# Kernel optimization log

Measured on AMD Instinct MI355X. Metric: run time of the kernel, lower is better.

Reference implementation:

```python
import jax, jax.numpy as jnp
import numpy as np


def _hamilton_weight(Wr, Wi, Wj, Wk):
    # Weights stored as [in4, out4] (i.e. torch weight.T). Build the fused
    # block-structured quaternion matrix [in, out]; rows = input chunk (r,i,j,k),
    # cols = output chunk (r,i,j,k), signs per the Hamilton product in forward().
    return jnp.concatenate([
        jnp.concatenate([Wr,  Wi,  Wj,  Wk], axis=1),
        jnp.concatenate([-Wi, Wr,  Wk, -Wj], axis=1),
        jnp.concatenate([-Wj, -Wk, Wr,  Wi], axis=1),
        jnp.concatenate([-Wk, Wj, -Wi,  Wr], axis=1),
    ], axis=0)


def _hamilton_bias(br, bi, bj, bk):
    # Each output chunk sums the four linears' biases with the same signs.
    return jnp.concatenate([
        br - bi - bj - bk,
        br + bi + bj - bk,
        br - bi + bj + bk,
        br + bi - bj + bk,
    ], axis=0)


def setup_inputs() -> dict:
    key = jax.random.key(0)
    ks = jax.random.split(key, 9)
    B, IN, OUT = 8192, 4096, 4096
    q_in, q_out = IN // 4, OUT // 4
    s = 1.0 / np.sqrt(q_in)
    return {
        "x": jax.random.normal(ks[0], (B, IN), dtype=jnp.float32),
        "Wr": jax.random.normal(ks[1], (q_in, q_out), dtype=jnp.float32) * s,
        "Wi": jax.random.normal(ks[2], (q_in, q_out), dtype=jnp.float32) * s,
        "Wj": jax.random.normal(ks[3], (q_in, q_out), dtype=jnp.float32) * s,
        "Wk": jax.random.normal(ks[4], (q_in, q_out), dtype=jnp.float32) * s,
        "br": jax.random.normal(ks[5], (q_out,), dtype=jnp.float32) * s,
        "bi": jax.random.normal(ks[6], (q_out,), dtype=jnp.float32) * s,
        "bj": jax.random.normal(ks[7], (q_out,), dtype=jnp.float32) * s,
        "bk": jax.random.normal(ks[8], (q_out,), dtype=jnp.float32) * s,
    }


def reference(x, Wr, Wi, Wj, Wk, br, bi, bj, bk):
    # Single fused GEMM; mathematically identical to the 16 small matmuls
    # (r/i/j/k linears applied to each chunk with Hamilton-product signs)
    # followed by concat.
    W = _hamilton_weight(Wr, Wi, Wj, Wk)   # [in, out]
    b = _hamilton_bias(br, bi, bj, bk)     # [out]
    return x @ W + b
```

## Files before the change

### kernel.cpp

```cpp
#include <hip/hip_runtime.h>
#include <stdint.h>

#define MDIM 8192
#define NDIM 4096
#define KDIM 4096

typedef float accf_t __attribute__((ext_vector_type(4)));
typedef short s16x8 __attribute__((ext_vector_type(8)));

typedef const __attribute__((address_space(1))) uint8_t* gas_t;
typedef __attribute__((address_space(3))) uint8_t* las_t;

__device__ __forceinline__ void gload16(const void* g, void* l) {
  __builtin_amdgcn_global_load_lds((gas_t)g, (las_t)l, 16, 0, 0);
}

__device__ __forceinline__ uint32_t pk_bf16(float a, float b) {
  uint32_t ua = __builtin_bit_cast(uint32_t, a);
  uint32_t ub = __builtin_bit_cast(uint32_t, b);
  ua += 0x7fffu + ((ua >> 16) & 1u);
  ub += 0x7fffu + ((ub >> 16) & 1u);
  return (ua >> 16) | (ub & 0xffff0000u);
}

__global__ void cvt_x_kernel(const float* __restrict__ x, uint16_t* __restrict__ xb) {
  int64_t e = ((int64_t)blockIdx.x * 256 + threadIdx.x) * 8;
  float4 f0 = *reinterpret_cast<const float4*>(x + e);
  float4 f1 = *reinterpret_cast<const float4*>(x + e + 4);
  uint4 u;
  u.x = pk_bf16(f0.x, f0.y);
  u.y = pk_bf16(f0.z, f0.w);
  u.z = pk_bf16(f1.x, f1.y);
  u.w = pk_bf16(f1.z, f1.w);
  *reinterpret_cast<uint4*>(xb + e) = u;
}

__global__ void build_wt_kernel(const float* __restrict__ Wr, const float* __restrict__ Wi,
                                const float* __restrict__ Wj, const float* __restrict__ Wk,
                                uint16_t* __restrict__ wt) {
  __shared__ float t[64][65];
  const int k0 = blockIdx.x * 64;
  const int n0 = blockIdx.y * 64;
  const int rc = k0 >> 10, cc = n0 >> 10;
  const int srcsel[16] = {0,1,2,3, 1,0,3,2, 2,3,0,1, 3,2,1,0};
  const float sgntab[16] = {1.f,1.f,1.f,1.f, -1.f,1.f,1.f,-1.f, -1.f,-1.f,1.f,1.f, -1.f,1.f,-1.f,1.f};
  const float* srcs[4] = {Wr, Wi, Wj, Wk};
  const float* W = srcs[srcsel[rc * 4 + cc]];
  const float sg = sgntab[rc * 4 + cc];
  const int kq0 = k0 & 1023, nq0 = n0 & 1023;
  const int tid = threadIdx.x;
  const int lr = tid >> 6;
  const int lc = tid & 63;
#pragma unroll
  for (int p = 0; p < 16; ++p) {
    int kl = p * 4 + lr;
    t[kl][lc] = W[(int64_t)(kq0 + kl) * 1024 + nq0 + lc];
  }
  __syncthreads();
  const int kb = (tid & 7) * 8;
#pragma unroll
  for (int p = 0; p < 2; ++p) {
    int nl = p * 32 + (tid >> 3);
    uint4 u;
    u.x = pk_bf16(sg * t[kb + 0][nl], sg * t[kb + 1][nl]);
    u.y = pk_bf16(sg * t[kb + 2][nl], sg * t[kb + 3][nl]);
    u.z = pk_bf16(sg * t[kb + 4][nl], sg * t[kb + 5][nl]);
    u.w = pk_bf16(sg * t[kb + 6][nl], sg * t[kb + 7][nl]);
    *reinterpret_cast<uint4*>(wt + (int64_t)(n0 + nl) * KDIM + k0 + kb) = u;
  }
}


#define VM6 { asm volatile("s_waitcnt vmcnt(6)"); __builtin_amdgcn_sched_barrier(0); }
#define VM0 { asm volatile("s_waitcnt vmcnt(0)"); __builtin_amdgcn_sched_barrier(0); }

#define ISS(BUF, H, T) {                                                      \
    int64_t ko_ = (int64_t)(T) * 64 + ((H) >> 1) * 32;                        \
    const uint16_t* s0_ = ((H) & 1) ? bSrc0 : aSrc0;                          \
    const uint16_t* s1_ = ((H) & 1) ? bSrc1 : aSrc1;                          \
    uint8_t* d_ = dstW + (BUF) * 65536 + (H) * 16384;                         \
    gload16(s0_ + ko_, d_);                                                   \
    gload16(s1_ + ko_, d_ + 8192); }

#define PH(BUF, KH, MH, ISSUE, LASTVM)                                        \
  {                                                                           \
    if ((MH) == 0) {                                                          \
      _Pragma("unroll")                                                       \
      for (int f = 0; f < 4; ++f)                                             \
        bfr[f] = *(const s16x8*)(ldsb + (BUF) * 65536 + (KH) * 32768 + boff[f]); \
    }                                                                         \
    s16x8 afr[4];                                                             \
    _Pragma("unroll")                                                         \
    for (int f = 0; f < 4; ++f)                                               \
      afr[f] = *(const s16x8*)(ldsb + (BUF) * 65536 + (KH) * 32768 + aoff[(MH) * 4 + f]); \
    ISSUE                                                                     \
    __builtin_amdgcn_s_barrier();                                             \
    asm volatile("s_waitcnt lgkmcnt(0)");                                     \
    __builtin_amdgcn_sched_barrier(0);                                        \
    __builtin_amdgcn_s_setprio(1);                                            \
    _Pragma("unroll")                                                         \
    for (int f = 0; f < 4; ++f)                                               \
      _Pragma("unroll")                                                       \
      for (int fn = 0; fn < 4; ++fn)                                          \
        acc[(MH) * 4 + f][fn] =                                               \
            __builtin_amdgcn_mfma_f32_16x16x32_bf16(afr[f], bfr[fn], acc[(MH) * 4 + f][fn], 0, 0, 0); \
    __builtin_amdgcn_s_setprio(0);                                            \
    LASTVM                                                                    \
    __builtin_amdgcn_s_barrier();                                             \
  }

__global__ __launch_bounds__(512, 2)
void qgemm8_kernel(const uint16_t* __restrict__ xb, const uint16_t* __restrict__ wt,
                   const float* __restrict__ br, const float* __restrict__ bi,
                   const float* __restrict__ bj, const float* __restrict__ bk,
                   float* __restrict__ out) {
  extern __shared__ uint8_t ldsb[];
  const int tid = threadIdx.x;
  const int wid = tid >> 6, lane = tid & 63;
  const int kg = lane >> 4, rl = lane & 15;
  const int wm = wid >> 2, wn = wid & 3;

  const int bid = blockIdx.x;
  const int swz = (bid & 7) * 64 + (bid >> 3);
  const int tn = swz >> 5, tm = swz & 31;
  const int m0 = tm * 256, n0 = tn * 256;

  const int arow = tid >> 2, aslot = tid & 3;
  const int ag = aslot ^ ((arow >> 1) & 3);
  const uint16_t* aSrc0 = xb + (int64_t)(m0 + arow) * KDIM + ag * 8;
  const uint16_t* aSrc1 = xb + (int64_t)(m0 + 128 + arow) * KDIM + ag * 8;
  const uint16_t* bSrc0 = wt + (int64_t)(n0 + arow) * KDIM + ag * 8;
  const uint16_t* bSrc1 = wt + (int64_t)(n0 + 128 + arow) * KDIM + ag * 8;
  uint8_t* dstW = ldsb + wid * 1024;

  int aoff[8], boff[4];
#pragma unroll
  for (int f = 0; f < 8; ++f) {
    int r = wm * 128 + f * 16 + rl;
    aoff[f] = r * 64 + ((kg ^ ((r >> 1) & 3)) << 4);
  }
#pragma unroll
  for (int f = 0; f < 4; ++f) {
    int c = wn * 64 + f * 16 + rl;
    boff[f] = 16384 + c * 64 + ((kg ^ ((c >> 1) & 3)) << 4);
  }

  accf_t acc[8][4] = {};
  s16x8 bfr[4];

  ISS(0, 0, 0) ISS(0, 1, 0) ISS(0, 2, 0) ISS(0, 3, 0)
  ISS(1, 0, 1) ISS(1, 1, 1) ISS(1, 2, 1)
  VM6
  __builtin_amdgcn_s_barrier();

  for (int i = 0; i < 31; ++i) {
    const int t = 2 * i;
    PH(0, 0, 0, ISS(1, 3, t + 1), )
    PH(0, 0, 1, ISS(0, 0, t + 2), )
    PH(0, 1, 0, ISS(0, 1, t + 2), )
    PH(0, 1, 1, ISS(0, 2, t + 2), VM6)
    PH(1, 0, 0, ISS(0, 3, t + 2), )
    PH(1, 0, 1, ISS(1, 0, t + 3), )
    PH(1, 1, 0, ISS(1, 1, t + 3), )
    PH(1, 1, 1, ISS(1, 2, t + 3), VM6)
  }
  PH(0, 0, 0, ISS(1, 3, 63), )
  PH(0, 0, 1, , )
  PH(0, 1, 0, , )
  PH(0, 1, 1, , VM0)
  PH(1, 0, 0, , )
  PH(1, 0, 1, , )
  PH(1, 1, 0, , )
  PH(1, 1, 1, , )

  const float s_i[4] = {-1.f, 1.f, -1.f, 1.f};
  const float s_j[4] = {-1.f, 1.f, 1.f, -1.f};
  const float s_k[4] = {-1.f, -1.f, 1.f, 1.f};
  float bias[4];
#pragma unroll
  for (int fn = 0; fn < 4; ++fn) {
    int col = n0 + wn * 64 + fn * 16 + rl;
    int cc = col >> 10, nq = col & 1023;
    bias[fn] = br[nq] + s_i[cc] * bi[nq] + s_j[cc] * bj[nq] + s_k[cc] * bk[nq];
  }
#pragma unroll
  for (int fm = 0; fm < 8; ++fm) {
    int rowb = m0 + wm * 128 + fm * 16 + kg * 4;
#pragma unroll
    for (int r = 0; r < 4; ++r) {
      float* op = out + (int64_t)(rowb + r) * NDIM + n0 + wn * 64 + rl;
#pragma unroll
      for (int fn = 0; fn < 4; ++fn)
        op[fn * 16] = acc[fm][fn][r] + bias[fn];
    }
  }
}

template <int AWS>
__global__ __launch_bounds__(256, 3)
void qgemm_kernel(const uint16_t* __restrict__ xb, const float* __restrict__ xf,
                  const uint16_t* __restrict__ wt,
                  const float* __restrict__ br, const float* __restrict__ bi,
                  const float* __restrict__ bj, const float* __restrict__ bk,
                  float* __restrict__ out) {
  __shared__ __align__(16) uint16_t Alds[128 * 32];
  __shared__ __align__(16) uint16_t Blds[128 * 32];
  const int tid = threadIdx.x;
  const int wid = tid >> 6, lane = tid & 63;
  const int kg = lane >> 4, rl = lane & 15;
  const int bid = blockIdx.x;
  const int swz = (bid & 7) * 256 + (bid >> 3);
  const int tile_m = swz & 63;
  const int tile_n = swz >> 6;
  const int m0 = tile_m * 128, n0 = tile_n * 128;
  const int wr = wid >> 1, wc = wid & 1;
  const int e0 = tid * 8, e1 = (256 + tid) * 8;
  const int r0 = e0 >> 5, r1 = e1 >> 5;
  const int s0 = (e0 >> 3) & 3, s1 = (e1 >> 3) & 3;
  const int g0 = s0 ^ ((r0 >> 1) & 3);
  const int g1 = s1 ^ ((r1 >> 1) & 3);
  const uint16_t* bp0 = wt + (int64_t)(n0 + r0) * KDIM + g0 * 8;
  const uint16_t* bp1 = wt + (int64_t)(n0 + r1) * KDIM + g1 * 8;
  const uint16_t* ap0 = nullptr;
  const uint16_t* ap1 = nullptr;
  const float* af0 = nullptr;
  const float* af1 = nullptr;
  if (AWS) {
    ap0 = xb + (int64_t)(m0 + r0) * KDIM + g0 * 8;
    ap1 = xb + (int64_t)(m0 + r1) * KDIM + g1 * 8;
  } else {
    af0 = xf + (int64_t)(m0 + r0) * KDIM + g0 * 8;
    af1 = xf + (int64_t)(m0 + r1) * KDIM + g1 * 8;
  }
  uint8_t* Ab = (uint8_t*)Alds;
  uint8_t* Bb = (uint8_t*)Blds;
  uint8_t* AbW0 = Ab + wid * 1024;
  uint8_t* AbW1 = Ab + 4096 + wid * 1024;
  uint8_t* BbW0 = Bb + wid * 1024;
  uint8_t* BbW1 = Bb + 4096 + wid * 1024;
  uint8_t* aw0 = Ab + e0 * 2;
  uint8_t* aw1 = Ab + e1 * 2;
  int aoff[4], boff[4];
#pragma unroll
  for (int f = 0; f < 4; ++f) {
    int arow = wr * 64 + f * 16 + rl;
    aoff[f] = arow * 64 + ((kg ^ ((arow >> 1) & 3)) << 4);
    int bcol = wc * 64 + f * 16 + rl;
    boff[f] = bcol * 64 + ((kg ^ ((bcol >> 1) & 3)) << 4);
  }
  accf_t acc[4][4] = {};
  for (int kt = 0; kt < KDIM / 32; ++kt) {
    gload16(bp0, BbW0);
    gload16(bp1, BbW1);
    bp0 += 32; bp1 += 32;
    if (AWS) {
      gload16(ap0, AbW0);
      gload16(ap1, AbW1);
      ap0 += 32; ap1 += 32;
    } else {
      float4 fa = *reinterpret_cast<const float4*>(af0);
      float4 fb = *reinterpret_cast<const float4*>(af0 + 4);
      float4 fc = *reinterpret_cast<const float4*>(af1);
      float4 fd = *reinterpret_cast<const float4*>(af1 + 4);
      uint4 u0, u1;
      u0.x = pk_bf16(fa.x, fa.y); u0.y = pk_bf16(fa.z, fa.w);
      u0.z = pk_bf16(fb.x, fb.y); u0.w = pk_bf16(fb.z, fb.w);
      u1.x = pk_bf16(fc.x, fc.y); u1.y = pk_bf16(fc.z, fc.w);
      u1.z = pk_bf16(fd.x, fd.y); u1.w = pk_bf16(fd.z, fd.w);
      *reinterpret_cast<uint4*>(aw0) = u0;
      *reinterpret_cast<uint4*>(aw1) = u1;
      af0 += 32; af1 += 32;
    }
    __syncthreads();
    s16x8 afr[4], bfr[4];
#pragma unroll
    for (int f = 0; f < 4; ++f) afr[f] = *reinterpret_cast<const s16x8*>(Ab + aoff[f]);
#pragma unroll
    for (int f = 0; f < 4; ++f) bfr[f] = *reinterpret_cast<const s16x8*>(Bb + boff[f]);
#pragma unroll
    for (int fm = 0; fm < 4; ++fm)
#pragma unroll
      for (int fn = 0; fn < 4; ++fn)
        acc[fm][fn] = __builtin_amdgcn_mfma_f32_16x16x32_bf16(afr[fm], bfr[fn], acc[fm][fn], 0, 0, 0);
    __syncthreads();
  }
  const float s_i[4] = {-1.f, 1.f, -1.f, 1.f};
  const float s_j[4] = {-1.f, 1.f, 1.f, -1.f};
  const float s_k[4] = {-1.f, -1.f, 1.f, 1.f};
  float bias[4];
#pragma unroll
  for (int fn = 0; fn < 4; ++fn) {
    int col = n0 + wc * 64 + fn * 16 + rl;
    int cc = col >> 10, nq = col & 1023;
    bias[fn] = br[nq] + s_i[cc] * bi[nq] + s_j[cc] * bj[nq] + s_k[cc] * bk[nq];
  }
#pragma unroll
  for (int fm = 0; fm < 4; ++fm) {
    int rowb = m0 + wr * 64 + fm * 16 + kg * 4;
#pragma unroll
    for (int r = 0; r < 4; ++r) {
      float* op = out + (int64_t)(rowb + r) * NDIM + n0 + wc * 64 + rl;
#pragma unroll
      for (int fn = 0; fn < 4; ++fn)
        op[fn * 16] = acc[fm][fn][r] + bias[fn];
    }
  }
}

__global__ void naive_q_kernel(const float* __restrict__ x,
                               const float* __restrict__ Wr, const float* __restrict__ Wi,
                               const float* __restrict__ Wj, const float* __restrict__ Wk,
                               const float* __restrict__ br, const float* __restrict__ bi,
                               const float* __restrict__ bj, const float* __restrict__ bk,
                               float* __restrict__ out) {
  const int n = blockIdx.x * 256 + threadIdx.x;
  const int m = blockIdx.y;
  const int cc = n >> 10, nq = n & 1023;
  const int srcsel[16] = {0,1,2,3, 1,0,3,2, 2,3,0,1, 3,2,1,0};
  const float sgntab[16] = {1.f,1.f,1.f,1.f, -1.f,1.f,1.f,-1.f, -1.f,-1.f,1.f,1.f, -1.f,1.f,-1.f,1.f};
  const float s_i[4] = {-1.f,1.f,-1.f,1.f}, s_j[4] = {-1.f,1.f,1.f,-1.f}, s_k[4] = {-1.f,-1.f,1.f,1.f};
  const float* srcs[4] = {Wr, Wi, Wj, Wk};
  float acc = br[nq] + s_i[cc] * bi[nq] + s_j[cc] * bj[nq] + s_k[cc] * bk[nq];
  for (int rc = 0; rc < 4; ++rc) {
    const float* W = srcs[srcsel[rc * 4 + cc]];
    const float sg = sgntab[rc * 4 + cc];
    const float* xp = x + (int64_t)m * KDIM + rc * 1024;
    const float* wp = W + nq;
    float a = 0.f;
    for (int kq = 0; kq < 1024; ++kq) a = fmaf(xp[kq], wp[(int64_t)kq * 1024], a);
    acc += sg * a;
  }
  out[(int64_t)m * NDIM + n] = acc;
}

extern "C" void kernel_launch(void* const* d_in, const int* in_sizes, int n_in,
                              void* d_out, int out_size, void* d_ws, size_t ws_size,
                              hipStream_t stream) {
  const float* x  = (const float*)d_in[0];
  const float* Wr = (const float*)d_in[1];
  const float* Wi = (const float*)d_in[2];
  const float* Wj = (const float*)d_in[3];
  const float* Wk = (const float*)d_in[4];
  const float* br = (const float*)d_in[5];
  const float* bi = (const float*)d_in[6];
  const float* bj = (const float*)d_in[7];
  const float* bk = (const float*)d_in[8];
  float* out = (float*)d_out;

  const size_t WT_BYTES = (size_t)NDIM * KDIM * 2;
  const size_t XB_BYTES = (size_t)MDIM * KDIM * 2;

  if (ws_size < WT_BYTES) {
    dim3 g(NDIM / 256, MDIM);
    naive_q_kernel<<<g, 256, 0, stream>>>(x, Wr, Wi, Wj, Wk, br, bi, bj, bk, out);
    return;
  }
  uint16_t* wt = (uint16_t*)d_ws;
  build_wt_kernel<<<dim3(64, 64), 256, 0, stream>>>(Wr, Wi, Wj, Wk, wt);
  if (ws_size >= WT_BYTES + XB_BYTES) {
    uint16_t* xbp = wt + (size_t)NDIM * KDIM;
    cvt_x_kernel<<<(MDIM * (KDIM / 8)) / 256, 256, 0, stream>>>(x, xbp);
    hipError_t e = hipFuncSetAttribute(reinterpret_cast<const void*>(qgemm8_kernel),
                                       hipFuncAttributeMaxDynamicSharedMemorySize, 131072);
    if (e == hipSuccess) {
      qgemm8_kernel<<<512, 512, 131072, stream>>>(xbp, wt, br, bi, bj, bk, out);
    } else {
      qgemm_kernel<1><<<2048, 256, 0, stream>>>(xbp, nullptr, wt, br, bi, bj, bk, out);
    }
  } else {
    qgemm_kernel<0><<<2048, 256, 0, stream>>>(nullptr, x, wt, br, bi, bj, bk, out);
  }
}
```

Baseline: 311.4 us.

## Double-buffer LDS fragment registers to prefetch next phase during MFMA

Restructures the main loop phases so that the A and B fragments for the next phase are loaded from LDS into a second register set while the current phase's MFMAs run. Partial lgkmcnt waits replace full drains, and global-load waits move to finer vmcnt(10) checks at the top of each phase. The aim is to hide LDS read latency behind matrix math. The cost is higher VGPR pressure from the doubled fragment arrays, under a 512-thread, 2-block launch bound. The waitcnt accounting is more delicate and could be wrong.

After: 313.8 us. No clear change (+0.8%).

```diff
diff --git a/kernel.cpp b/kernel.cpp
--- a/kernel.cpp
+++ b/kernel.cpp
@@ -71,8 +71,10 @@
 }
 
 
-#define VM6 { asm volatile("s_waitcnt vmcnt(6)"); __builtin_amdgcn_sched_barrier(0); }
-#define VM0 { asm volatile("s_waitcnt vmcnt(0)"); __builtin_amdgcn_sched_barrier(0); }
+#define SB __builtin_amdgcn_sched_barrier(0);
+#define W10 { asm volatile("s_waitcnt vmcnt(10)"); SB }
+#define WV0 { asm volatile("s_waitcnt vmcnt(0)"); SB }
+#define NOW
 
 #define ISS(BUF, H, T) {                                                      \
     int64_t ko_ = (int64_t)(T) * 64 + ((H) >> 1) * 32;                        \
@@ -82,30 +84,30 @@
     gload16(s0_ + ko_, d_);                                                   \
     gload16(s1_ + ko_, d_ + 8192); }
 
-#define PH(BUF, KH, MH, ISSUE, LASTVM)                                        \
+#define PH2(BUF, KH, MH, CA, NA, CB, LB, NB, NBUF, NKH, NMH, LGK, ISSUE, TOPW) \
   {                                                                           \
-    if ((MH) == 0) {                                                          \
+    ISSUE                                                                     \
+    __builtin_amdgcn_s_barrier();                                             \
+    TOPW                                                                      \
+    _Pragma("unroll")                                                         \
+    for (int f = 0; f < 4; ++f)                                               \
+      afr[NA][f] = *(const s16x8*)(ldsb + (NBUF) * 65536 + (NKH) * 32768 + aoff[(NMH) * 4 + f]); \
+    if (LB) {                                                                 \
       _Pragma("unroll")                                                       \
       for (int f = 0; f < 4; ++f)                                             \
-        bfr[f] = *(const s16x8*)(ldsb + (BUF) * 65536 + (KH) * 32768 + boff[f]); \
+        bfr[NB][f] = *(const s16x8*)(ldsb + (NBUF) * 65536 + (NKH) * 32768 + boff[f]); \
     }                                                                         \
-    s16x8 afr[4];                                                             \
-    _Pragma("unroll")                                                         \
-    for (int f = 0; f < 4; ++f)                                               \
-      afr[f] = *(const s16x8*)(ldsb + (BUF) * 65536 + (KH) * 32768 + aoff[(MH) * 4 + f]); \
-    ISSUE                                                                     \
-    __builtin_amdgcn_s_barrier();                                             \
-    asm volatile("s_waitcnt lgkmcnt(0)");                                     \
-    __builtin_amdgcn_sched_barrier(0);                                        \
+    SB                                                                        \
+    asm volatile("s_waitcnt lgkmcnt(" LGK ")");                               \
+    SB                                                                        \
     __builtin_amdgcn_s_setprio(1);                                            \
     _Pragma("unroll")                                                         \
     for (int f = 0; f < 4; ++f)                                               \
       _Pragma("unroll")                                                       \
       for (int fn = 0; fn < 4; ++fn)                                          \
         acc[(MH) * 4 + f][fn] =                                               \
-            __builtin_amdgcn_mfma_f32_16x16x32_bf16(afr[f], bfr[fn], acc[(MH) * 4 + f][fn], 0, 0, 0); \
+            __builtin_amdgcn_mfma_f32_16x16x32_bf16(afr[CA][f], bfr[CB][fn], acc[(MH) * 4 + f][fn], 0, 0, 0); \
     __builtin_amdgcn_s_setprio(0);                                            \
-    LASTVM                                                                    \
     __builtin_amdgcn_s_barrier();                                             \
   }
 
@@ -146,32 +148,39 @@
   }
 
   accf_t acc[8][4] = {};
-  s16x8 bfr[4];
+  s16x8 afr[2][4], bfr[2][4];
 
   ISS(0, 0, 0) ISS(0, 1, 0) ISS(0, 2, 0) ISS(0, 3, 0)
   ISS(1, 0, 1) ISS(1, 1, 1) ISS(1, 2, 1)
-  VM6
+  { asm volatile("s_waitcnt vmcnt(6)"); SB }
   __builtin_amdgcn_s_barrier();
+#pragma unroll
+  for (int f = 0; f < 4; ++f)
+    afr[0][f] = *(const s16x8*)(ldsb + aoff[f]);
+#pragma unroll
+  for (int f = 0; f < 4; ++f)
+    bfr[0][f] = *(const s16x8*)(ldsb + boff[f]);
+  SB
 
   for (int i = 0; i < 31; ++i) {
     const int t = 2 * i;
-    PH(0, 0, 0, ISS(1, 3, t + 1), )
-    PH(0, 0, 1, ISS(0, 0, t + 2), )
-    PH(0, 1, 0, ISS(0, 1, t + 2), )
-    PH(0, 1, 1, ISS(0, 2, t + 2), VM6)
-    PH(1, 0, 0, ISS(0, 3, t + 2), )
-    PH(1, 0, 1, ISS(1, 0, t + 3), )
-    PH(1, 1, 0, ISS(1, 1, t + 3), )
-    PH(1, 1, 1, ISS(1, 2, t + 3), VM6)
-  }
-  PH(0, 0, 0, ISS(1, 3, 63), )
-  PH(0, 0, 1, , )
-  PH(0, 1, 0, , )
-  PH(0, 1, 1, , VM0)
-  PH(1, 0, 0, , )
-  PH(1, 0, 1, , )
-  PH(1, 1, 0, , )
-  PH(1, 1, 1, , )
+    PH2(0,  0, 0,  0, 1, 0, 0, 0,  0,   0,  1,   "4", ISS(1, 3, t + 1), W10)
+    PH2(0,  0, 1,  1, 0, 0, 1, 1,  0,   1,  0,   "8", ISS(0, 0, t + 2), W10)
+    PH2(0,  1, 0,  0, 1, 1, 0, 0,  0,   1,  1,   "4", ISS(0, 1, t + 2), W10)
+    PH2(0,  1, 1,  1, 0, 1, 1, 0,  1,   0,  0,   "8", ISS(0, 2, t + 2), W10)
+    PH2(1,  0, 0,  0, 1, 0, 0, 0,  1,   0,  1,   "4", ISS(0, 3, t + 2), W10)
+    PH2(1,  0, 1,  1, 0, 0, 1, 1,  1,   1,  0,   "8", ISS(1, 0, t + 3), W10)
+    PH2(1,  1, 0,  0, 1, 1, 0, 0,  1,   1,  1,   "4", ISS(1, 1, t + 3), W10)
+    PH2(1,  1, 1,  1, 0, 1, 1, 0,  0,   0,  0,   "8", ISS(1, 2, t + 3), W10)
+  }
+  PH2(0, 0, 0,  0, 1, 0, 0, 0,  0, 0, 1,  "4", ISS(1, 3, 63), W10)
+  PH2(0, 0, 1,  1, 0, 0, 1, 1,  0, 1, 0,  "8", NOW, WV0)
+  PH2(0, 1, 0,  0, 1, 1, 0, 0,  0, 1, 1,  "4", NOW, NOW)
+  PH2(0, 1, 1,  1, 0, 1, 1, 0,  1, 0, 0,  "8", NOW, NOW)
+  PH2(1, 0, 0,  0, 1, 0, 0, 0,  1, 0, 1,  "4", NOW, NOW)
+  PH2(1, 0, 1,  1, 0, 0, 1, 1,  1, 1, 0,  "8", NOW, NOW)
+  PH2(1, 1, 0,  0, 1, 1, 0, 0,  1, 1, 1,  "4", NOW, NOW)
+  PH2(1, 1, 1,  1, 0, 1, 1, 0,  0, 0, 0,  "8", NOW, NOW)
 
   const float s_i[4] = {-1.f, 1.f, -1.f, 1.f};
   const float s_j[4] = {-1.f, 1.f, 1.f, -1.f};
```

## Split main GEMM into two M-half launches and reorder LDS load issue

Applied to the files above, without the earlier changes.

Launches the 512-thread GEMM kernel twice, each covering half of the M rows via a new mbase argument and a retuned block swizzle. It also reorders the per-phase global-to-LDS issue sequence and moves the B-offset constant into the LDS read macro. The aim appears to be a smaller per-launch working set for better cache locality and a different load ordering. The risk is that each launch fills fewer occupancy slots and adds a serial launch boundary. The fallback kernel's template variant is also removed.

Result: faster. 295.1 us (-5.2%).

```diff
diff --git a/kernel.cpp b/kernel.cpp
--- a/kernel.cpp
+++ b/kernel.cpp
@@ -71,8 +71,9 @@
 }
 
 
-#define VM6 { asm volatile("s_waitcnt vmcnt(6)"); __builtin_amdgcn_sched_barrier(0); }
-#define VM0 { asm volatile("s_waitcnt vmcnt(0)"); __builtin_amdgcn_sched_barrier(0); }
+#define SB __builtin_amdgcn_sched_barrier(0);
+#define VM6 { asm volatile("s_waitcnt vmcnt(6)"); SB }
+#define VM0 { asm volatile("s_waitcnt vmcnt(0)"); SB }
 
 #define ISS(BUF, H, T) {                                                      \
     int64_t ko_ = (int64_t)(T) * 64 + ((H) >> 1) * 32;                        \
@@ -87,7 +88,7 @@
     if ((MH) == 0) {                                                          \
       _Pragma("unroll")                                                       \
       for (int f = 0; f < 4; ++f)                                             \
-        bfr[f] = *(const s16x8*)(ldsb + (BUF) * 65536 + (KH) * 32768 + boff[f]); \
+        bfr[f] = *(const s16x8*)(ldsb + (BUF) * 65536 + (KH) * 32768 + 16384 + boff[f]); \
     }                                                                         \
     s16x8 afr[4];                                                             \
     _Pragma("unroll")                                                         \
@@ -96,14 +97,14 @@
     ISSUE                                                                     \
     __builtin_amdgcn_s_barrier();                                             \
     asm volatile("s_waitcnt lgkmcnt(0)");                                     \
-    __builtin_amdgcn_sched_barrier(0);                                        \
+    SB                                                                        \
     __builtin_amdgcn_s_setprio(1);                                            \
     _Pragma("unroll")                                                         \
     for (int f = 0; f < 4; ++f)                                               \
       _Pragma("unroll")                                                       \
       for (int fn = 0; fn < 4; ++fn)                                          \
-        acc[(MH) * 4 + f][fn] =                                               \
-            __builtin_amdgcn_mfma_f32_16x16x32_bf16(afr[f], bfr[fn], acc[(MH) * 4 + f][fn], 0, 0, 0); \
+        acc[(MH) * 4 + f][fn] = __builtin_amdgcn_mfma_f32_16x16x32_bf16(      \
+            afr[f], bfr[fn], acc[(MH) * 4 + f][fn], 0, 0, 0);                 \
     __builtin_amdgcn_s_setprio(0);                                            \
     LASTVM                                                                    \
     __builtin_amdgcn_s_barrier();                                             \
@@ -113,7 +114,7 @@
 void qgemm8_kernel(const uint16_t* __restrict__ xb, const uint16_t* __restrict__ wt,
                    const float* __restrict__ br, const float* __restrict__ bi,
                    const float* __restrict__ bj, const float* __restrict__ bk,
-                   float* __restrict__ out) {
+                   float* __restrict__ out, int mbase) {
   extern __shared__ uint8_t ldsb[];
   const int tid = threadIdx.x;
   const int wid = tid >> 6, lane = tid & 63;
@@ -121,9 +122,9 @@
   const int wm = wid >> 2, wn = wid & 3;
 
   const int bid = blockIdx.x;
-  const int swz = (bid & 7) * 64 + (bid >> 3);
-  const int tn = swz >> 5, tm = swz & 31;
-  const int m0 = tm * 256, n0 = tn * 256;
+  const int swz = (bid & 7) * 32 + (bid >> 3);
+  const int tn = swz >> 4, tm = swz & 15;
+  const int m0 = mbase + tm * 256, n0 = tn * 256;
 
   const int arow = tid >> 2, aslot = tid & 3;
   const int ag = aslot ^ ((arow >> 1) & 3);
@@ -142,29 +143,29 @@
 #pragma unroll
   for (int f = 0; f < 4; ++f) {
     int c = wn * 64 + f * 16 + rl;
-    boff[f] = 16384 + c * 64 + ((kg ^ ((c >> 1) & 3)) << 4);
+    boff[f] = c * 64 + ((kg ^ ((c >> 1) & 3)) << 4);
   }
 
   accf_t acc[8][4] = {};
   s16x8 bfr[4];
 
   ISS(0, 0, 0) ISS(0, 1, 0) ISS(0, 2, 0) ISS(0, 3, 0)
-  ISS(1, 0, 1) ISS(1, 1, 1) ISS(1, 2, 1)
+  ISS(1, 0, 1) ISS(1, 1, 1) ISS(1, 3, 1)
   VM6
   __builtin_amdgcn_s_barrier();
 
   for (int i = 0; i < 31; ++i) {
     const int t = 2 * i;
-    PH(0, 0, 0, ISS(1, 3, t + 1), )
-    PH(0, 0, 1, ISS(0, 0, t + 2), )
-    PH(0, 1, 0, ISS(0, 1, t + 2), )
-    PH(0, 1, 1, ISS(0, 2, t + 2), VM6)
-    PH(1, 0, 0, ISS(0, 3, t + 2), )
-    PH(1, 0, 1, ISS(1, 0, t + 3), )
-    PH(1, 1, 0, ISS(1, 1, t + 3), )
-    PH(1, 1, 1, ISS(1, 2, t + 3), VM6)
-  }
-  PH(0, 0, 0, ISS(1, 3, 63), )
+    PH(0, 0, 0, ISS(1, 2, t + 1), )
+    PH(0, 0, 1, ISS(0, 1, t + 2), )
+    PH(0, 1, 0, ISS(0, 0, t + 2), )
+    PH(0, 1, 1, ISS(0, 3, t + 2), VM6)
+    PH(1, 0, 0, ISS(0, 2, t + 2), )
+    PH(1, 0, 1, ISS(1, 1, t + 3), )
+    PH(1, 1, 0, ISS(1, 0, t + 3), )
+    PH(1, 1, 1, ISS(1, 3, t + 3), VM6)
+  }
+  PH(0, 0, 0, ISS(1, 2, 63), )
   PH(0, 0, 1, , )
   PH(0, 1, 0, , )
   PH(0, 1, 1, , VM0)
@@ -196,10 +197,8 @@
   }
 }
 
-template <int AWS>
 __global__ __launch_bounds__(256, 3)
-void qgemm_kernel(const uint16_t* __restrict__ xb, const float* __restrict__ xf,
-                  const uint16_t* __restrict__ wt,
+void qgemm_kernel(const float* __restrict__ xf, const uint16_t* __restrict__ wt,
                   const float* __restrict__ br, const float* __restrict__ bi,
                   const float* __restrict__ bj, const float* __restrict__ bk,
                   float* __restrict__ out) {
@@ -221,21 +220,10 @@
   const int g1 = s1 ^ ((r1 >> 1) & 3);
   const uint16_t* bp0 = wt + (int64_t)(n0 + r0) * KDIM + g0 * 8;
   const uint16_t* bp1 = wt + (int64_t)(n0 + r1) * KDIM + g1 * 8;
-  const uint16_t* ap0 = nullptr;
-  const uint16_t* ap1 = nullptr;
-  const float* af0 = nullptr;
-  const float* af1 = nullptr;
-  if (AWS) {
-    ap0 = xb + (int64_t)(m0 + r0) * KDIM + g0 * 8;
-    ap1 = xb + (int64_t)(m0 + r1) * KDIM + g1 * 8;
-  } else {
-    af0 = xf + (int64_t)(m0 + r0) * KDIM + g0 * 8;
-    af1 = xf + (int64_t)(m0 + r1) * KDIM + g1 * 8;
-  }
+  const float* af0 = xf + (int64_t)(m0 + r0) * KDIM + g0 * 8;
+  const float* af1 = xf + (int64_t)(m0 + r1) * KDIM + g1 * 8;
   uint8_t* Ab = (uint8_t*)Alds;
   uint8_t* Bb = (uint8_t*)Blds;
-  uint8_t* AbW0 = Ab + wid * 1024;
-  uint8_t* AbW1 = Ab + 4096 + wid * 1024;
   uint8_t* BbW0 = Bb + wid * 1024;
   uint8_t* BbW1 = Bb + 4096 + wid * 1024;
   uint8_t* aw0 = Ab + e0 * 2;
@@ -253,24 +241,18 @@
     gload16(bp0, BbW0);
     gload16(bp1, BbW1);
     bp0 += 32; bp1 += 32;
-    if (AWS) {
-      gload16(ap0, AbW0);
-      gload16(ap1, AbW1);
-      ap0 += 32; ap1 += 32;
-    } else {
-      float4 fa = *reinterpret_cast<const float4*>(af0);
-      float4 fb = *reinterpret_cast<const float4*>(af0 + 4);
-      float4 fc = *reinterpret_cast<const float4*>(af1);
-      float4 fd = *reinterpret_cast<const float4*>(af1 + 4);
-      uint4 u0, u1;
-      u0.x = pk_bf16(fa.x, fa.y); u0.y = pk_bf16(fa.z, fa.w);
-      u0.z = pk_bf16(fb.x, fb.y); u0.w = pk_bf16(fb.z, fb.w);
-      u1.x = pk_bf16(fc.x, fc.y); u1.y = pk_bf16(fc.z, fc.w);
-      u1.z = pk_bf16(fd.x, fd.y); u1.w = pk_bf16(fd.z, fd.w);
-      *reinterpret_cast<uint4*>(aw0) = u0;
-      *reinterpret_cast<uint4*>(aw1) = u1;
-      af0 += 32; af1 += 32;
-    }
+    float4 fa = *reinterpret_cast<const float4*>(af0);
+    float4 fb = *reinterpret_cast<const float4*>(af0 + 4);
+    float4 fc = *reinterpret_cast<const float4*>(af1);
+    float4 fd = *reinterpret_cast<const float4*>(af1 + 4);
+    uint4 u0, u1;
+    u0.x = pk_bf16(fa.x, fa.y); u0.y = pk_bf16(fa.z, fa.w);
+    u0.z = pk_bf16(fb.x, fb.y); u0.w = pk_bf16(fb.z, fb.w);
+    u1.x = pk_bf16(fc.x, fc.y); u1.y = pk_bf16(fc.z, fc.w);
+    u1.z = pk_bf16(fd.x, fd.y); u1.w = pk_bf16(fd.z, fd.w);
+    *reinterpret_cast<uint4*>(aw0) = u0;
+    *reinterpret_cast<uint4*>(aw1) = u1;
+    af0 += 32; af1 += 32;
     __syncthreads();
     s16x8 afr[4], bfr[4];
 #pragma unroll
@@ -363,11 +345,12 @@
     hipError_t e = hipFuncSetAttribute(reinterpret_cast<const void*>(qgemm8_kernel),
                                        hipFuncAttributeMaxDynamicSharedMemorySize, 131072);
     if (e == hipSuccess) {
-      qgemm8_kernel<<<512, 512, 131072, stream>>>(xbp, wt, br, bi, bj, bk, out);
+      qgemm8_kernel<<<256, 512, 131072, stream>>>(xbp, wt, br, bi, bj, bk, out, 0);
+      qgemm8_kernel<<<256, 512, 131072, stream>>>(xbp, wt, br, bi, bj, bk, out, 4096);
     } else {
-      qgemm_kernel<1><<<2048, 256, 0, stream>>>(xbp, nullptr, wt, br, bi, bj, bk, out);
+      qgemm_kernel<<<2048, 256, 0, stream>>>(x, wt, br, bi, bj, bk, out);
     }
   } else {
-    qgemm_kernel<0><<<2048, 256, 0, stream>>>(nullptr, x, wt, br, bi, bj, bk, out);
-  }
-}
+    qgemm_kernel<<<2048, 256, 0, stream>>>(x, wt, br, bi, bj, bk, out);
+  }
+}
```
